# Kernel optimization log

Hardware: AMD Instinct MI355X
Metric: run time of the kernel (lower is better)

## Reference

```python
import jax, jax.numpy as jnp
import numpy as np

EMBED_DIM = 1024
NUM_HEADS = 16
HEAD_DIM = EMBED_DIM // NUM_HEADS
B, QL, KVL = 2, 2048, 2048


def setup_inputs() -> dict:
    key = jax.random.key(0)
    ks = jax.random.split(key, 16)
    std = 0.02
    inp = {
        "query": jax.random.normal(ks[0], (B, QL, EMBED_DIM), jnp.float32),
        "key": jax.random.normal(ks[1], (B, KVL, EMBED_DIM), jnp.float32),
        "value": jax.random.normal(ks[2], (B, KVL, EMBED_DIM), jnp.float32),
        "logit_scale": jax.random.uniform(ks[3], (1,), jnp.float32),
        "logit_bias": jax.random.normal(ks[4], (1,), jnp.float32),
        "Wq": jax.random.normal(ks[5], (EMBED_DIM, EMBED_DIM), jnp.float32) * std,
        "bq": jnp.zeros((EMBED_DIM,), jnp.float32),
        "Wk": jax.random.normal(ks[6], (EMBED_DIM, EMBED_DIM), jnp.float32) * std,
        "bk": jnp.zeros((EMBED_DIM,), jnp.float32),
        "Wv": jax.random.normal(ks[7], (EMBED_DIM, EMBED_DIM), jnp.float32) * std,
        "bv": jnp.zeros((EMBED_DIM,), jnp.float32),
        "Wo": jax.random.normal(ks[8], (EMBED_DIM, EMBED_DIM), jnp.float32) * std,
        "bo": jnp.zeros((EMBED_DIM,), jnp.float32),
    }
    return inp


def reference(query, key, value, logit_scale, logit_bias, Wq, bq, Wk, bk, Wv, bv, Wo, bo):
    # projections (torch Linear: x @ W.T + b)
    q = query @ Wq.T + bq    # [B, QL, D]
    k = key @ Wk.T + bk      # [B, KVL, D]
    v = value @ Wv.T + bv    # [B, KVL, D]

    # QK L2-normalization over the FULL embed_dim (before head split), per source
    q = q / jnp.linalg.norm(q, axis=-1, keepdims=True)
    k = k / jnp.linalg.norm(k, axis=-1, keepdims=True)
    scale = jnp.exp(logit_scale)  # [1], broadcasts
    bias = logit_bias             # [1], broadcasts

    # split heads: [B, H, L, Dh]
    qh = q.reshape(B, QL, NUM_HEADS, HEAD_DIM).transpose(0, 2, 1, 3)
    kh = k.reshape(B, KVL, NUM_HEADS, HEAD_DIM).transpose(0, 2, 1, 3)
    vh = v.reshape(B, KVL, NUM_HEADS, HEAD_DIM).transpose(0, 2, 1, 3)

    scores = jnp.einsum("bhqd,bhkd->bhqk", qh, kh) * scale + bias  # [B,H,QL,KVL]
    attn = jax.nn.softmax(scores.astype(jnp.float32), axis=-1).astype(qh.dtype)
    # dropout p=0.0 -> identity
    out = jnp.einsum("bhqk,bhkd->bhqd", attn, vh)  # [B,H,QL,Dh]
    out = out.transpose(0, 2, 1, 3).reshape(B, QL, EMBED_DIM)
    out = out @ Wo.T + bo
    return out, attn
```

## Files before the change

kernel.cpp:

```cpp
#include <hip/hip_runtime.h>

#define B_   2
#define L_   2048
#define D_   1024
#define H_   16
#define DH_  64
#define M_TOT (B_ * L_)

typedef __attribute__((ext_vector_type(8))) __bf16 bf16x8;
typedef __attribute__((ext_vector_type(4))) float f32x4;
typedef __attribute__((ext_vector_type(8))) unsigned short u16x8;

__device__ __forceinline__ unsigned short f2bf(float f) {
    unsigned int u = __float_as_uint(f);
    u += 0x7fffu + ((u >> 16) & 1u);
    return (unsigned short)(u >> 16);
}
__device__ __forceinline__ float bf2f(unsigned short u) {
    return __uint_as_float(((unsigned int)u) << 16);
}

__device__ __forceinline__ void gload_lds16(const void* g, void* l) {
    __builtin_amdgcn_global_load_lds(
        (__attribute__((address_space(1))) void*)(void*)g,
        (__attribute__((address_space(3))) void*)l, 16, 0, 0);
}

__global__ __launch_bounds__(256) void cast_in(const float* __restrict__ src,
                                               u16x8* __restrict__ dst)
{
    const int i = blockIdx.x * 256 + threadIdx.x;
    const float4* s = (const float4*)src;
    float4 a = s[2 * i], b = s[2 * i + 1];
    u16x8 w;
    w[0] = f2bf(a.x); w[1] = f2bf(a.y); w[2] = f2bf(a.z); w[3] = f2bf(a.w);
    w[4] = f2bf(b.x); w[5] = f2bf(b.y); w[6] = f2bf(b.z); w[7] = f2bf(b.w);
    dst[i] = w;
}

__global__ __launch_bounds__(256) void cast_w4(const float* __restrict__ Wq,
                                               const float* __restrict__ Wk,
                                               const float* __restrict__ Wv,
                                               const float* __restrict__ Wo,
                                               u16x8* __restrict__ dst)
{
    const int y = blockIdx.y;
    const float* src = (y == 0) ? Wq : (y == 1) ? Wk : (y == 2) ? Wv : Wo;
    const int i = blockIdx.x * 256 + threadIdx.x;
    const float4* s = (const float4*)src;
    float4 a = s[2 * i], b = s[2 * i + 1];
    u16x8 w;
    w[0] = f2bf(a.x); w[1] = f2bf(a.y); w[2] = f2bf(a.z); w[3] = f2bf(a.w);
    w[4] = f2bf(b.x); w[5] = f2bf(b.y); w[6] = f2bf(b.z); w[7] = f2bf(b.w);
    dst[(size_t)y * (D_ * D_ / 8) + i] = w;
}

template<bool F32OUT>
__global__ __launch_bounds__(256, 3) void gemm_nt_mfma(
    const unsigned short* __restrict__ A, const unsigned short* __restrict__ W,
    const float* __restrict__ bias, void* __restrict__ Cout, int K, int N)
{
    __shared__ __align__(16) unsigned short As[2][128 * 64];
    __shared__ __align__(16) unsigned short Bs[2][64 * 64];
    const int tid  = threadIdx.x;
    const int bm   = blockIdx.x * 128;
    const int bn   = blockIdx.y * 64;
    const int lane = tid & 63, wid = tid >> 6;
    const int wm   = (wid >> 1) * 64, wn = (wid & 1) * 32;
    const int kg   = lane >> 4, lr = lane & 15;
    const int swz  = lr & 7;

    f32x4 zero = {0.f, 0.f, 0.f, 0.f};
    f32x4 acc[4][2];
    #pragma unroll
    for (int m = 0; m < 4; ++m) { acc[m][0] = zero; acc[m][1] = zero; }

    #pragma unroll
    for (int i = 0; i < 4; ++i) {
        int c = i * 256 + tid, row = c >> 3, c8 = (c & 7) ^ (row & 7);
        gload_lds16(A + (size_t)(bm + row) * K + c8 * 8, (char*)As[0] + c * 16);
    }
    #pragma unroll
    for (int i = 0; i < 2; ++i) {
        int c = i * 256 + tid, row = c >> 3, c8 = (c & 7) ^ (row & 7);
        gload_lds16(W + (size_t)(bn + row) * K + c8 * 8, (char*)Bs[0] + c * 16);
    }

    const int nIt = K / 64;
    int cur = 0;
    for (int it = 0; it < nIt; ++it) {
        __syncthreads();
        if (it + 1 < nIt) {
            const int k0 = (it + 1) * 64;
            #pragma unroll
            for (int i = 0; i < 4; ++i) {
                int c = i * 256 + tid, row = c >> 3, c8 = (c & 7) ^ (row & 7);
                gload_lds16(A + (size_t)(bm + row) * K + k0 + c8 * 8,
                            (char*)As[cur ^ 1] + c * 16);
            }
            #pragma unroll
            for (int i = 0; i < 2; ++i) {
                int c = i * 256 + tid, row = c >> 3, c8 = (c & 7) ^ (row & 7);
                gload_lds16(W + (size_t)(bn + row) * K + k0 + c8 * 8,
                            (char*)Bs[cur ^ 1] + c * 16);
            }
        }
        #pragma unroll
        for (int ks = 0; ks < 2; ++ks) {
            bf16x8 af[4], bfr[2];
            #pragma unroll
            for (int m = 0; m < 4; ++m)
                af[m] = *(const bf16x8*)((const char*)As[cur] +
                        (wm + m * 16 + lr) * 128 + (((ks * 4 + kg) ^ swz) << 4));
            #pragma unroll
            for (int n = 0; n < 2; ++n)
                bfr[n] = *(const bf16x8*)((const char*)Bs[cur] +
                        (wn + n * 16 + lr) * 128 + (((ks * 4 + kg) ^ swz) << 4));
            #pragma unroll
            for (int m = 0; m < 4; ++m)
                #pragma unroll
                for (int n = 0; n < 2; ++n)
                    acc[m][n] = __builtin_amdgcn_mfma_f32_16x16x32_bf16(
                        af[m], bfr[n], acc[m][n], 0, 0, 0);
        }
        cur ^= 1;
    }

    #pragma unroll
    for (int n = 0; n < 2; ++n) {
        const int col = bn + wn + n * 16 + lr;
        const float bv = bias[col];
        #pragma unroll
        for (int m = 0; m < 4; ++m) {
            const int row0 = bm + wm + m * 16 + kg * 4;
            #pragma unroll
            for (int r = 0; r < 4; ++r) {
                float val = acc[m][n][r] + bv;
                if (F32OUT)
                    ((float*)Cout)[(size_t)(row0 + r) * N + col] = val;
                else
                    ((unsigned short*)Cout)[(size_t)(row0 + r) * N + col] = f2bf(val);
            }
        }
    }
}

__global__ __launch_bounds__(256, 3) void attn_sums(
    const unsigned short* __restrict__ qn, const unsigned short* __restrict__ kn,
    const float* __restrict__ ls, const float* __restrict__ lb,
    float* __restrict__ sums)
{
    __shared__ __align__(16) unsigned short Qs[128 * 64];
    __shared__ __align__(16) unsigned short Ks[2][128 * 64];
    __shared__ float red[2][128];
    const int flat = blockIdx.x;
    const int z  = (flat & 7) * 4 + ((flat >> 3) & 3);
    const int qt = flat >> 5;
    const int b = z >> 4, h = z & 15;
    const unsigned short* Qp = qn + (size_t)b * L_ * D_ + h * DH_;
    const unsigned short* Kp = kn + (size_t)b * L_ * D_ + h * DH_;

    const int tid = threadIdx.x;
    const int bm  = qt * 128;
    const int lane = tid & 63, wid = tid >> 6;
    const int wq = wid >> 1, wkv = wid & 1;
    const int kg = lane >> 4, lr = lane & 15;
    const int swz = lr & 7;

    #pragma unroll
    for (int i = 0; i < 4; ++i) {
        int c = i * 256 + tid, row = c >> 3, c8 = (c & 7) ^ (row & 7);
        gload_lds16(Qp + (size_t)(bm + row) * D_ + c8 * 8, (char*)Qs + c * 16);
    }
    #pragma unroll
    for (int i = 0; i < 4; ++i) {
        int c = i * 256 + tid, row = c >> 3, c8 = (c & 7) ^ (row & 7);
        gload_lds16(Kp + (size_t)row * D_ + c8 * 8, (char*)Ks[0] + c * 16);
    }

    const float scale = expf(ls[0]);
    const float sb = lb[0];
    f32x4 zero = {0.f, 0.f, 0.f, 0.f};
    float rs[4][4] = {};
    int cur = 0;

    for (int it = 0; it < L_ / 128; ++it) {
        __syncthreads();
        if (it + 1 < L_ / 128) {
            const int kv = (it + 1) * 128;
            #pragma unroll
            for (int i = 0; i < 4; ++i) {
                int c = i * 256 + tid, row = c >> 3, c8 = (c & 7) ^ (row & 7);
                gload_lds16(Kp + (size_t)(kv + row) * D_ + c8 * 8,
                            (char*)Ks[cur ^ 1] + c * 16);
            }
        }
        f32x4 s[4][4];
        #pragma unroll
        for (int m = 0; m < 4; ++m)
            #pragma unroll
            for (int n = 0; n < 4; ++n) s[m][n] = zero;
        #pragma unroll
        for (int ks = 0; ks < 2; ++ks) {
            bf16x8 af[4], bfr[4];
            #pragma unroll
            for (int m = 0; m < 4; ++m)
                af[m] = *(const bf16x8*)((const char*)Qs +
                        (wq * 64 + m * 16 + lr) * 128 + (((ks * 4 + kg) ^ swz) << 4));
            #pragma unroll
            for (int n = 0; n < 4; ++n)
                bfr[n] = *(const bf16x8*)((const char*)Ks[cur] +
                        (wkv * 64 + n * 16 + lr) * 128 + (((ks * 4 + kg) ^ swz) << 4));
            #pragma unroll
            for (int m = 0; m < 4; ++m)
                #pragma unroll
                for (int n = 0; n < 4; ++n)
                    s[m][n] = __builtin_amdgcn_mfma_f32_16x16x32_bf16(
                        af[m], bfr[n], s[m][n], 0, 0, 0);
        }
        #pragma unroll
        for (int m = 0; m < 4; ++m)
            #pragma unroll
            for (int n = 0; n < 4; ++n)
                #pragma unroll
                for (int r = 0; r < 4; ++r)
                    rs[m][r] += __expf(s[m][n][r] * scale + sb);
        cur ^= 1;
    }

    #pragma unroll
    for (int m = 0; m < 4; ++m)
        #pragma unroll
        for (int r = 0; r < 4; ++r) {
            float sv = rs[m][r];
            sv += __shfl_xor(sv, 1); sv += __shfl_xor(sv, 2);
            sv += __shfl_xor(sv, 4); sv += __shfl_xor(sv, 8);
            if (lr == 0) red[wkv][wq * 64 + m * 16 + kg * 4 + r] = sv;
        }
    __syncthreads();
    if (tid < 128)
        sums[(size_t)z * L_ + bm + tid] = red[0][tid] + red[1][tid];
}

__global__ __launch_bounds__(256, 3) void attn_fused(
    const unsigned short* __restrict__ qn, const unsigned short* __restrict__ kn,
    const unsigned short* __restrict__ Vt, const float* __restrict__ sums,
    const float* __restrict__ ls, const float* __restrict__ lb,
    float* __restrict__ attn, unsigned short* __restrict__ ctx)
{
    __shared__ __align__(16) unsigned short Qs[64 * 64];
    __shared__ __align__(16) unsigned short Ks[2][64 * 64];
    __shared__ __align__(16) unsigned short Vs[2][64 * 64];
    __shared__ __align__(16) unsigned short Ps[64 * 64];
    __shared__ float invs[64];
    const int flat = blockIdx.x;
    const int z  = (flat & 7) * 4 + ((flat >> 3) & 3);
    const int qt = flat >> 5;
    const int b = z >> 4, h = z & 15;
    const unsigned short* Qp = qn + (size_t)b * L_ * D_ + h * DH_;
    const unsigned short* Kp = kn + (size_t)b * L_ * D_ + h * DH_;
    const unsigned short* Vp = Vt + (size_t)z * DH_ * L_;
    float* Cp = attn + (size_t)z * L_ * L_;
    unsigned short* Op = ctx + (size_t)b * L_ * D_ + h * DH_;

    const int tid = threadIdx.x;
    const int bm  = qt * 64;
    const int lane = tid & 63, wid = tid >> 6;
    const int wq = wid >> 1, wkv = wid & 1;
    const int kg = lane >> 4, lr = lane & 15;
    const int swz = lr & 7;

    #pragma unroll
    for (int i = 0; i < 2; ++i) {
        int c = i * 256 + tid, row = c >> 3, c8 = (c & 7) ^ (row & 7);
        gload_lds16(Qp + (size_t)(bm + row) * D_ + c8 * 8, (char*)Qs + c * 16);
    }
    #pragma unroll
    for (int i = 0; i < 2; ++i) {
        int c = i * 256 + tid, row = c >> 3, c8 = (c & 7) ^ (row & 7);
        gload_lds16(Kp + (size_t)row * D_ + c8 * 8, (char*)Ks[0] + c * 16);
    }
    #pragma unroll
    for (int i = 0; i < 2; ++i) {
        int c = i * 256 + tid, row = c >> 3, c8 = (c & 7) ^ (row & 7);
        gload_lds16(Vp + (size_t)row * L_ + c8 * 8, (char*)Vs[0] + c * 16);
    }
    if (tid < 64) invs[tid] = 1.0f / sums[(size_t)z * L_ + bm + tid];

    const float scale = expf(ls[0]);
    const float sb = lb[0];
    f32x4 zero = {0.f, 0.f, 0.f, 0.f};
    f32x4 cacc[2][4];
    #pragma unroll
    for (int m = 0; m < 2; ++m)
        #pragma unroll
        for (int n = 0; n < 4; ++n) cacc[m][n] = zero;

    int cur = 0;
    for (int it = 0; it < L_ / 64; ++it) {
        __syncthreads();
        if (it + 1 < L_ / 64) {
            const int kv = (it + 1) * 64;
            #pragma unroll
            for (int i = 0; i < 2; ++i) {
                int c = i * 256 + tid, row = c >> 3, c8 = (c & 7) ^ (row & 7);
                gload_lds16(Kp + (size_t)(kv + row) * D_ + c8 * 8,
                            (char*)Ks[cur ^ 1] + c * 16);
            }
            #pragma unroll
            for (int i = 0; i < 2; ++i) {
                int c = i * 256 + tid, row = c >> 3, c8 = (c & 7) ^ (row & 7);
                gload_lds16(Vp + (size_t)row * L_ + kv + c8 * 8,
                            (char*)Vs[cur ^ 1] + c * 16);
            }
        }

        f32x4 s[2][2];
        #pragma unroll
        for (int m = 0; m < 2; ++m) { s[m][0] = zero; s[m][1] = zero; }
        #pragma unroll
        for (int ks = 0; ks < 2; ++ks) {
            bf16x8 af[2], bfr[2];
            #pragma unroll
            for (int m = 0; m < 2; ++m)
                af[m] = *(const bf16x8*)((const char*)Qs +
                        (wq * 32 + m * 16 + lr) * 128 + (((ks * 4 + kg) ^ swz) << 4));
            #pragma unroll
            for (int n = 0; n < 2; ++n)
                bfr[n] = *(const bf16x8*)((const char*)Ks[cur] +
                        (wkv * 32 + n * 16 + lr) * 128 + (((ks * 4 + kg) ^ swz) << 4));
            #pragma unroll
            for (int m = 0; m < 2; ++m)
                #pragma unroll
                for (int n = 0; n < 2; ++n)
                    s[m][n] = __builtin_amdgcn_mfma_f32_16x16x32_bf16(
                        af[m], bfr[n], s[m][n], 0, 0, 0);
        }

        const int kv0 = it * 64;
        #pragma unroll
        for (int m = 0; m < 2; ++m) {
            #pragma unroll
            for (int n = 0; n < 2; ++n) {
                #pragma unroll
                for (int r = 0; r < 4; ++r) {
                    const int row_l = wq * 32 + m * 16 + kg * 4 + r;
                    const int col_l = wkv * 32 + n * 16 + lr;
                    float e = __expf(s[m][n][r] * scale + sb) * invs[row_l];
                    Cp[(size_t)(bm + row_l) * L_ + kv0 + col_l] = e;
                    Ps[row_l * 64 + (((col_l >> 3) ^ (row_l & 7)) << 3) + (col_l & 7)]
                        = f2bf(e);
                }
            }
        }
        asm volatile("s_waitcnt lgkmcnt(0)" ::: "memory");
        __builtin_amdgcn_sched_barrier(0);

        {
            bf16x8 pa[2], vb[4];
            #pragma unroll
            for (int m = 0; m < 2; ++m)
                pa[m] = *(const bf16x8*)((const char*)Ps +
                        (wq * 32 + m * 16 + lr) * 128 + (((wkv * 4 + kg) ^ swz) << 4));
            #pragma unroll
            for (int n = 0; n < 4; ++n)
                vb[n] = *(const bf16x8*)((const char*)Vs[cur] +
                        (n * 16 + lr) * 128 + (((wkv * 4 + kg) ^ swz) << 4));
            #pragma unroll
            for (int m = 0; m < 2; ++m)
                #pragma unroll
                for (int n = 0; n < 4; ++n)
                    cacc[m][n] = __builtin_amdgcn_mfma_f32_16x16x32_bf16(
                        pa[m], vb[n], cacc[m][n], 0, 0, 0);
        }
        cur ^= 1;
    }

    __syncthreads();
    float* redp = (float*)Ks;
    if (wkv == 1) {
        #pragma unroll
        for (int m = 0; m < 2; ++m)
            #pragma unroll
            for (int n = 0; n < 4; ++n)
                #pragma unroll
                for (int r = 0; r < 4; ++r)
                    redp[(wq * 32 + m * 16 + kg * 4 + r) * 64 + n * 16 + lr]
                        = cacc[m][n][r];
    }
    __syncthreads();
    if (wkv == 0) {
        #pragma unroll
        for (int m = 0; m < 2; ++m) {
            #pragma unroll
            for (int n = 0; n < 4; ++n) {
                #pragma unroll
                for (int r = 0; r < 4; ++r) {
                    const int row_l = wq * 32 + m * 16 + kg * 4 + r;
                    const int col   = n * 16 + lr;
                    float val = cacc[m][n][r] + redp[row_l * 64 + col];
                    Op[(size_t)(bm + row_l) * D_ + col] = f2bf(val);
                }
            }
        }
    }
}

__global__ __launch_bounds__(256) void transpose_v(
    const unsigned short* __restrict__ v8, unsigned short* __restrict__ Vt)
{
    __shared__ unsigned short tile[64][66];
    const int z = blockIdx.y, b = z >> 4, h = z & 15;
    const int t0 = blockIdx.x * 64;
    const unsigned short* src = v8 + ((size_t)(b * L_ + t0)) * D_ + h * DH_;
    unsigned short* dst = Vt + (size_t)z * DH_ * L_ + t0;
    const int t = threadIdx.x;
    #pragma unroll
    for (int i = 0; i < 2; ++i) {
        int c = i * 256 + t;
        int r = c >> 3, c8 = c & 7;
        u16x8 v = *(const u16x8*)(src + (size_t)r * D_ + c8 * 8);
        #pragma unroll
        for (int e = 0; e < 8; ++e) tile[r][c8 * 8 + e] = v[e];
    }
    __syncthreads();
    #pragma unroll
    for (int i = 0; i < 2; ++i) {
        int c = i * 256 + t;
        int d = c >> 3, c8 = c & 7;
        u16x8 v;
        #pragma unroll
        for (int e = 0; e < 8; ++e) v[e] = tile[c8 * 8 + e][d];
        *(u16x8*)(dst + (size_t)d * L_ + c8 * 8) = v;
    }
}

__global__ __launch_bounds__(256) void l2norm2(unsigned short* __restrict__ q8,
                                               unsigned short* __restrict__ k8)
{
    unsigned short* base = blockIdx.y ? k8 : q8;
    unsigned short* row = base + (size_t)blockIdx.x * D_;
    const int tid = threadIdx.x;
    ushort4 v = ((ushort4*)row)[tid];
    float f0 = bf2f(v.x), f1 = bf2f(v.y), f2 = bf2f(v.z), f3 = bf2f(v.w);
    float ss = f0 * f0 + f1 * f1 + f2 * f2 + f3 * f3;
    #pragma unroll
    for (int off = 32; off >= 1; off >>= 1)
        ss += __shfl_xor(ss, off);
    __shared__ float red[4];
    const int lane = tid & 63, wid = tid >> 6;
    if (lane == 0) red[wid] = ss;
    __syncthreads();
    ss = red[0] + red[1] + red[2] + red[3];
    const float inv = rsqrtf(ss);
    ushort4 o;
    o.x = f2bf(f0 * inv); o.y = f2bf(f1 * inv);
    o.z = f2bf(f2 * inv); o.w = f2bf(f3 * inv);
    ((ushort4*)row)[tid] = o;
}

extern "C" void kernel_launch(void* const* d_in, const int* in_sizes, int n_in,
                              void* d_out, int out_size, void* d_ws, size_t ws_size,
                              hipStream_t stream)
{
    const float* query = (const float*)d_in[0];
    const float* key_  = (const float*)d_in[1];
    const float* value = (const float*)d_in[2];
    const float* ls    = (const float*)d_in[3];
    const float* lb    = (const float*)d_in[4];
    const float* Wq    = (const float*)d_in[5];
    const float* bq    = (const float*)d_in[6];
    const float* Wk    = (const float*)d_in[7];
    const float* bk    = (const float*)d_in[8];
    const float* Wv    = (const float*)d_in[9];
    const float* bv    = (const float*)d_in[10];
    const float* Wo    = (const float*)d_in[11];
    const float* bo    = (const float*)d_in[12];

    float* out  = (float*)d_out;
    float* attn = out + (size_t)M_TOT * D_;

    unsigned short* xb = (unsigned short*)d_ws;
    unsigned short* Wb = xb + (size_t)M_TOT * D_;
    unsigned short* q8 = Wb + (size_t)4 * D_ * D_;
    unsigned short* k8 = q8 + (size_t)M_TOT * D_;
    unsigned short* v8 = k8 + (size_t)M_TOT * D_;
    unsigned short* Vt = v8 + (size_t)M_TOT * D_;
    unsigned short* ctxb = xb;
    float* sums = (float*)v8;

    dim3 blk(256);
    const dim3 gproj(M_TOT / 128, D_ / 64);

    cast_w4<<<dim3(D_ * D_ / 8 / 256, 4), blk, 0, stream>>>(Wq, Wk, Wv, Wo, (u16x8*)Wb);

    cast_in<<<M_TOT * D_ / 8 / 256, blk, 0, stream>>>(query, (u16x8*)xb);
    gemm_nt_mfma<false><<<gproj, blk, 0, stream>>>(xb, Wb + 0 * (size_t)D_ * D_, bq, q8, D_, D_);
    cast_in<<<M_TOT * D_ / 8 / 256, blk, 0, stream>>>(key_, (u16x8*)xb);
    gemm_nt_mfma<false><<<gproj, blk, 0, stream>>>(xb, Wb + 1 * (size_t)D_ * D_, bk, k8, D_, D_);
    cast_in<<<M_TOT * D_ / 8 / 256, blk, 0, stream>>>(value, (u16x8*)xb);
    gemm_nt_mfma<false><<<gproj, blk, 0, stream>>>(xb, Wb + 2 * (size_t)D_ * D_, bv, v8, D_, D_);

    l2norm2<<<dim3(M_TOT, 2), blk, 0, stream>>>(q8, k8);

    transpose_v<<<dim3(L_ / 64, B_ * H_), blk, 0, stream>>>(v8, Vt);

    attn_sums<<<dim3(512), blk, 0, stream>>>(q8, k8, ls, lb, sums);

    attn_fused<<<dim3(1024), blk, 0, stream>>>(q8, k8, Vt, sums, ls, lb, attn, ctxb);

    gemm_nt_mfma<true><<<gproj, blk, 0, stream>>>(ctxb, Wb + 3 * (size_t)D_ * D_, bo, out, D_, D_);
}
```

Baseline: 801.2 us.

## Fuse fp32-to-bf16 input cast into batched QKV GEMM and merge norm/transpose kernels

The three separate cast+GEMM pairs for Q, K, V become one batched GEMM launch over a z-grid. That GEMM reads fp32 activations directly into registers, converts them to bf16 and writes them into swizzled LDS, so the intermediate bf16 activation buffer and its extra global round trip go away. The L2-norm and V-transpose kernels are merged into one launch. The cost is that A-tile loads now go through registers instead of async global-to-LDS copies, which may raise register pressure and reduce overlap. The fp32 A reads are also twice as wide as the old bf16 reads.

```diff
diff --git a/kernel.cpp b/kernel.cpp
--- a/kernel.cpp
+++ b/kernel.cpp
@@ -24,18 +24,6 @@
     __builtin_amdgcn_global_load_lds(
         (__attribute__((address_space(1))) void*)(void*)g,
         (__attribute__((address_space(3))) void*)l, 16, 0, 0);
-}
-
-__global__ __launch_bounds__(256) void cast_in(const float* __restrict__ src,
-                                               u16x8* __restrict__ dst)
-{
-    const int i = blockIdx.x * 256 + threadIdx.x;
-    const float4* s = (const float4*)src;
-    float4 a = s[2 * i], b = s[2 * i + 1];
-    u16x8 w;
-    w[0] = f2bf(a.x); w[1] = f2bf(a.y); w[2] = f2bf(a.z); w[3] = f2bf(a.w);
-    w[4] = f2bf(b.x); w[5] = f2bf(b.y); w[6] = f2bf(b.z); w[7] = f2bf(b.w);
-    dst[i] = w;
 }
 
 __global__ __launch_bounds__(256) void cast_w4(const float* __restrict__ Wq,
@@ -55,10 +43,129 @@
     dst[(size_t)y * (D_ * D_ / 8) + i] = w;
 }
 
-template<bool F32OUT>
-__global__ __launch_bounds__(256, 3) void gemm_nt_mfma(
+__global__ __launch_bounds__(256, 3) void gemm_qkv(
+    const float* __restrict__ Aq, const float* __restrict__ Ak,
+    const float* __restrict__ Av, const unsigned short* __restrict__ Wall,
+    const float* __restrict__ bq, const float* __restrict__ bk,
+    const float* __restrict__ bv,
+    unsigned short* __restrict__ q8, unsigned short* __restrict__ k8,
+    unsigned short* __restrict__ v8)
+{
+    __shared__ __align__(16) unsigned short As[2][128 * 64];
+    __shared__ __align__(16) unsigned short Bs[2][64 * 64];
+    const int z = blockIdx.z;
+    const float* A = (z == 0) ? Aq : (z == 1) ? Ak : Av;
+    const unsigned short* W = Wall + (size_t)z * D_ * D_;
+    const float* bias = (z == 0) ? bq : (z == 1) ? bk : bv;
+    unsigned short* C = (z == 0) ? q8 : (z == 1) ? k8 : v8;
+
+    const int tid  = threadIdx.x;
+    const int bm   = blockIdx.x * 128;
+    const int bn   = blockIdx.y * 64;
+    const int lane = tid & 63, wid = tid >> 6;
+    const int wm   = (wid >> 1) * 64, wn = (wid & 1) * 32;
+    const int kg   = lane >> 4, lr = lane & 15;
+    const int swz  = lr & 7;
+
+    f32x4 zero = {0.f, 0.f, 0.f, 0.f};
+    f32x4 acc[4][2];
+    #pragma unroll
+    for (int m = 0; m < 4; ++m) { acc[m][0] = zero; acc[m][1] = zero; }
+
+    float4 a0[4], a1[4];
+    #pragma unroll
+    for (int i = 0; i < 4; ++i) {
+        int c = i * 256 + tid, row = c >> 3, p = c & 7, c8 = p ^ (row & 7);
+        const float* src = A + (size_t)(bm + row) * D_ + c8 * 8;
+        a0[i] = *(const float4*)src;
+        a1[i] = *(const float4*)(src + 4);
+    }
+    #pragma unroll
+    for (int i = 0; i < 2; ++i) {
+        int c = i * 256 + tid, row = c >> 3, c8 = (c & 7) ^ (row & 7);
+        gload_lds16(W + (size_t)(bn + row) * D_ + c8 * 8, (char*)Bs[0] + c * 16);
+    }
+    #pragma unroll
+    for (int i = 0; i < 4; ++i) {
+        int c = i * 256 + tid, row = c >> 3, p = c & 7;
+        u16x8 w;
+        w[0] = f2bf(a0[i].x); w[1] = f2bf(a0[i].y);
+        w[2] = f2bf(a0[i].z); w[3] = f2bf(a0[i].w);
+        w[4] = f2bf(a1[i].x); w[5] = f2bf(a1[i].y);
+        w[6] = f2bf(a1[i].z); w[7] = f2bf(a1[i].w);
+        *(u16x8*)((char*)As[0] + row * 128 + (p << 4)) = w;
+    }
+
+    const int nIt = D_ / 64;
+    int cur = 0;
+    for (int it = 0; it < nIt; ++it) {
+        __syncthreads();
+        if (it + 1 < nIt) {
+            const int k0 = (it + 1) * 64;
+            #pragma unroll
+            for (int i = 0; i < 4; ++i) {
+                int c = i * 256 + tid, row = c >> 3, p = c & 7, c8 = p ^ (row & 7);
+                const float* src = A + (size_t)(bm + row) * D_ + k0 + c8 * 8;
+                a0[i] = *(const float4*)src;
+                a1[i] = *(const float4*)(src + 4);
+            }
+            #pragma unroll
+            for (int i = 0; i < 2; ++i) {
+                int c = i * 256 + tid, row = c >> 3, c8 = (c & 7) ^ (row & 7);
+                gload_lds16(W + (size_t)(bn + row) * D_ + k0 + c8 * 8,
+                            (char*)Bs[cur ^ 1] + c * 16);
+            }
+        }
+        #pragma unroll
+        for (int ks = 0; ks < 2; ++ks) {
+            bf16x8 af[4], bfr[2];
+            #pragma unroll
+            for (int m = 0; m < 4; ++m)
+                af[m] = *(const bf16x8*)((const char*)As[cur] +
+                        (wm + m * 16 + lr) * 128 + (((ks * 4 + kg) ^ swz) << 4));
+            #pragma unroll
+            for (int n = 0; n < 2; ++n)
+                bfr[n] = *(const bf16x8*)((const char*)Bs[cur] +
+                        (wn + n * 16 + lr) * 128 + (((ks * 4 + kg) ^ swz) << 4));
+            #pragma unroll
+            for (int m = 0; m < 4; ++m)
+                #pragma unroll
+                for (int n = 0; n < 2; ++n)
+                    acc[m][n] = __builtin_amdgcn_mfma_f32_16x16x32_bf16(
+                        af[m], bfr[n], acc[m][n], 0, 0, 0);
+        }
+        if (it + 1 < nIt) {
+            #pragma unroll
+            for (int i = 0; i < 4; ++i) {
+                int c = i * 256 + tid, row = c >> 3, p = c & 7;
+                u16x8 w;
+                w[0] = f2bf(a0[i].x); w[1] = f2bf(a0[i].y);
+                w[2] = f2bf(a0[i].z); w[3] = f2bf(a0[i].w);
+                w[4] = f2bf(a1[i].x); w[5] = f2bf(a1[i].y);
+                w[6] = f2bf(a1[i].z); w[7] = f2bf(a1[i].w);
+                *(u16x8*)((char*)As[cur ^ 1] + row * 128 + (p << 4)) = w;
+            }
+        }
+        cur ^= 1;
+    }
+
+    #pragma unroll
+    for (int n = 0; n < 2; ++n) {
+        const int col = bn + wn + n * 16 + lr;
+        const float bv_ = bias[col];
+        #pragma unroll
+        for (int m = 0; m < 4; ++m) {
+            const int row0 = bm + wm + m * 16 + kg * 4;
+            #pragma unroll
+            for (int r = 0; r < 4; ++r)
+                C[(size_t)(row0 + r) * D_ + col] = f2bf(acc[m][n][r] + bv_);
+        }
+    }
+}
+
+__global__ __launch_bounds__(256, 3) void gemm_out(
     const unsigned short* __restrict__ A, const unsigned short* __restrict__ W,
-    const float* __restrict__ bias, void* __restrict__ Cout, int K, int N)
+    const float* __restrict__ bias, float* __restrict__ Cout)
 {
     __shared__ __align__(16) unsigned short As[2][128 * 64];
     __shared__ __align__(16) unsigned short Bs[2][64 * 64];
@@ -78,15 +185,15 @@
     #pragma unroll
     for (int i = 0; i < 4; ++i) {
         int c = i * 256 + tid, row = c >> 3, c8 = (c & 7) ^ (row & 7);
-        gload_lds16(A + (size_t)(bm + row) * K + c8 * 8, (char*)As[0] + c * 16);
+        gload_lds16(A + (size_t)(bm + row) * D_ + c8 * 8, (char*)As[0] + c * 16);
     }
     #pragma unroll
     for (int i = 0; i < 2; ++i) {
         int c = i * 256 + tid, row = c >> 3, c8 = (c & 7) ^ (row & 7);
-        gload_lds16(W + (size_t)(bn + row) * K + c8 * 8, (char*)Bs[0] + c * 16);
-    }
-
-    const int nIt = K / 64;
+        gload_lds16(W + (size_t)(bn + row) * D_ + c8 * 8, (char*)Bs[0] + c * 16);
+    }
+
+    const int nIt = D_ / 64;
     int cur = 0;
     for (int it = 0; it < nIt; ++it) {
         __syncthreads();
@@ -95,13 +202,13 @@
             #pragma unroll
             for (int i = 0; i < 4; ++i) {
                 int c = i * 256 + tid, row = c >> 3, c8 = (c & 7) ^ (row & 7);
-                gload_lds16(A + (size_t)(bm + row) * K + k0 + c8 * 8,
+                gload_lds16(A + (size_t)(bm + row) * D_ + k0 + c8 * 8,
                             (char*)As[cur ^ 1] + c * 16);
             }
             #pragma unroll
             for (int i = 0; i < 2; ++i) {
                 int c = i * 256 + tid, row = c >> 3, c8 = (c & 7) ^ (row & 7);
-                gload_lds16(W + (size_t)(bn + row) * K + k0 + c8 * 8,
+                gload_lds16(W + (size_t)(bn + row) * D_ + k0 + c8 * 8,
                             (char*)Bs[cur ^ 1] + c * 16);
             }
         }
@@ -129,19 +236,70 @@
     #pragma unroll
     for (int n = 0; n < 2; ++n) {
         const int col = bn + wn + n * 16 + lr;
-        const float bv = bias[col];
+        const float bv_ = bias[col];
         #pragma unroll
         for (int m = 0; m < 4; ++m) {
             const int row0 = bm + wm + m * 16 + kg * 4;
             #pragma unroll
-            for (int r = 0; r < 4; ++r) {
-                float val = acc[m][n][r] + bv;
-                if (F32OUT)
-                    ((float*)Cout)[(size_t)(row0 + r) * N + col] = val;
-                else
-                    ((unsigned short*)Cout)[(size_t)(row0 + r) * N + col] = f2bf(val);
-            }
-        }
+            for (int r = 0; r < 4; ++r)
+                Cout[(size_t)(row0 + r) * D_ + col] = acc[m][n][r] + bv_;
+        }
+    }
+}
+
+__global__ __launch_bounds__(256) void norm_trans(
+    unsigned short* __restrict__ q8, unsigned short* __restrict__ k8,
+    const unsigned short* __restrict__ v8, unsigned short* __restrict__ Vt)
+{
+    __shared__ float red[4];
+    __shared__ unsigned short tile[64][66];
+    const int y = blockIdx.y;
+    const int tid = threadIdx.x;
+
+    if (y < 2) {
+        unsigned short* row = (y ? k8 : q8) + (size_t)blockIdx.x * D_;
+        ushort4 v = ((ushort4*)row)[tid];
+        float f0 = bf2f(v.x), f1 = bf2f(v.y), f2 = bf2f(v.z), f3 = bf2f(v.w);
+        float ss = f0 * f0 + f1 * f1 + f2 * f2 + f3 * f3;
+        #pragma unroll
+        for (int off = 32; off >= 1; off >>= 1)
+            ss += __shfl_xor(ss, off);
+        const int lane = tid & 63, wid = tid >> 6;
+        if (lane == 0) red[wid] = ss;
+        __syncthreads();
+        ss = red[0] + red[1] + red[2] + red[3];
+        const float inv = rsqrtf(ss);
+        ushort4 o;
+        o.x = f2bf(f0 * inv); o.y = f2bf(f1 * inv);
+        o.z = f2bf(f2 * inv); o.w = f2bf(f3 * inv);
+        ((ushort4*)row)[tid] = o;
+        return;
+    }
+
+    const int x = blockIdx.x;
+    if (x >= (L_ / 64) * (B_ * H_) / 32 * 32 || x >= 1024) return;
+    const int zz = x & 31, xt = x >> 5;
+    const int b = zz >> 4, h = zz & 15;
+    const int t0 = xt * 64;
+    const unsigned short* src = v8 + ((size_t)(b * L_ + t0)) * D_ + h * DH_;
+    unsigned short* dst = Vt + (size_t)zz * DH_ * L_ + t0;
+    #pragma unroll
+    for (int i = 0; i < 2; ++i) {
+        int c = i * 256 + tid;
+        int r = c >> 3, c8 = c & 7;
+        u16x8 v = *(const u16x8*)(src + (size_t)r * D_ + c8 * 8);
+        #pragma unroll
+        for (int e = 0; e < 8; ++e) tile[r][c8 * 8 + e] = v[e];
+    }
+    __syncthreads();
+    #pragma unroll
+    for (int i = 0; i < 2; ++i) {
+        int c = i * 256 + tid;
+        int d = c >> 3, c8 = c & 7;
+        u16x8 v;
+        #pragma unroll
+        for (int e = 0; e < 8; ++e) v[e] = tile[c8 * 8 + e][d];
+        *(u16x8*)(dst + (size_t)d * L_ + c8 * 8) = v;
     }
 }
 
@@ -406,59 +564,6 @@
     }
 }
 
-__global__ __launch_bounds__(256) void transpose_v(
-    const unsigned short* __restrict__ v8, unsigned short* __restrict__ Vt)
-{
-    __shared__ unsigned short tile[64][66];
-    const int z = blockIdx.y, b = z >> 4, h = z & 15;
-    const int t0 = blockIdx.x * 64;
-    const unsigned short* src = v8 + ((size_t)(b * L_ + t0)) * D_ + h * DH_;
-    unsigned short* dst = Vt + (size_t)z * DH_ * L_ + t0;
-    const int t = threadIdx.x;
-    #pragma unroll
-    for (int i = 0; i < 2; ++i) {
-        int c = i * 256 + t;
-        int r = c >> 3, c8 = c & 7;
-        u16x8 v = *(const u16x8*)(src + (size_t)r * D_ + c8 * 8);
-        #pragma unroll
-        for (int e = 0; e < 8; ++e) tile[r][c8 * 8 + e] = v[e];
-    }
-    __syncthreads();
-    #pragma unroll
-    for (int i = 0; i < 2; ++i) {
-        int c = i * 256 + t;
-        int d = c >> 3, c8 = c & 7;
-        u16x8 v;
-        #pragma unroll
-        for (int e = 0; e < 8; ++e) v[e] = tile[c8 * 8 + e][d];
-        *(u16x8*)(dst + (size_t)d * L_ + c8 * 8) = v;
-    }
-}
-
-__global__ __launch_bounds__(256) void l2norm2(unsigned short* __restrict__ q8,
-                                               unsigned short* __restrict__ k8)
-{
-    unsigned short* base = blockIdx.y ? k8 : q8;
-    unsigned short* row = base + (size_t)blockIdx.x * D_;
-    const int tid = threadIdx.x;
-    ushort4 v = ((ushort4*)row)[tid];
-    float f0 = bf2f(v.x), f1 = bf2f(v.y), f2 = bf2f(v.z), f3 = bf2f(v.w);
-    float ss = f0 * f0 + f1 * f1 + f2 * f2 + f3 * f3;
-    #pragma unroll
-    for (int off = 32; off >= 1; off >>= 1)
-        ss += __shfl_xor(ss, off);
-    __shared__ float red[4];
-    const int lane = tid & 63, wid = tid >> 6;
-    if (lane == 0) red[wid] = ss;
-    __syncthreads();
-    ss = red[0] + red[1] + red[2] + red[3];
-    const float inv = rsqrtf(ss);
-    ushort4 o;
-    o.x = f2bf(f0 * inv); o.y = f2bf(f1 * inv);
-    o.z = f2bf(f2 * inv); o.w = f2bf(f3 * inv);
-    ((ushort4*)row)[tid] = o;
-}
-
 extern "C" void kernel_launch(void* const* d_in, const int* in_sizes, int n_in,
                               void* d_out, int out_size, void* d_ws, size_t ws_size,
                               hipStream_t stream)
@@ -490,24 +595,18 @@
     float* sums = (float*)v8;
 
     dim3 blk(256);
-    const dim3 gproj(M_TOT / 128, D_ / 64);
 
     cast_w4<<<dim3(D_ * D_ / 8 / 256, 4), blk, 0, stream>>>(Wq, Wk, Wv, Wo, (u16x8*)Wb);
 
-    cast_in<<<M_TOT * D_ / 8 / 256, blk, 0, stream>>>(query, (u16x8*)xb);
-    gemm_nt_mfma<false><<<gproj, blk, 0, stream>>>(xb, Wb + 0 * (size_t)D_ * D_, bq, q8, D_, D_);
-    cast_in<<<M_TOT * D_ / 8 / 256, blk, 0, stream>>>(key_, (u16x8*)xb);
-    gemm_nt_mfma<false><<<gproj, blk, 0, stream>>>(xb, Wb + 1 * (size_t)D_ * D_, bk, k8, D_, D_);
-    cast_in<<<M_TOT * D_ / 8 / 256, blk, 0, stream>>>(value, (u16x8*)xb);
-    gemm_nt_mfma<false><<<gproj, blk, 0, stream>>>(xb, Wb + 2 * (size_t)D_ * D_, bv, v8, D_, D_);
-
-    l2norm2<<<dim3(M_TOT, 2), blk, 0, stream>>>(q8, k8);
-
-    transpose_v<<<dim3(L_ / 64, B_ * H_), blk, 0, stream>>>(v8, Vt);
+    gemm_qkv<<<dim3(M_TOT / 128, D_ / 64, 3), blk, 0, stream>>>(
+        query, key_, value, Wb, bq, bk, bv, q8, k8, v8);
+
+    norm_trans<<<dim3(M_TOT, 3), blk, 0, stream>>>(q8, k8, v8, Vt);
 
     attn_sums<<<dim3(512), blk, 0, stream>>>(q8, k8, ls, lb, sums);
 
     attn_fused<<<dim3(1024), blk, 0, stream>>>(q8, k8, Vt, sums, ls, lb, attn, ctxb);
 
-    gemm_nt_mfma<true><<<gproj, blk, 0, stream>>>(ctxb, Wb + 3 * (size_t)D_ * D_, bo, out, D_, D_);
-}
+    gemm_out<<<dim3(M_TOT / 128, D_ / 64), blk, 0, stream>>>(
+        ctxb, Wb + 3 * (size_t)D_ * D_, bo, out);
+}
```

New measurement: 812.2 us. About the same (+1.4%).
